# Performance work log

Measured on AMD Instinct MI355X. Metric: run time of the kernel, lower is better.

## Reference

```python
import jax, jax.numpy as jnp
import numpy as np

H_BINS = 64
SIGMA = 0.02
EPS = 1e-6


def setup_inputs() -> dict:
    key = jax.random.key(0)
    x = jax.random.uniform(key, (8, 3, 256, 256), dtype=jnp.float32)
    return {"x": x}


def reference(x):
    h = H_BINS
    L = x.shape[0]
    x = jnp.clip(x, 0.0, 1.0)
    I = x.reshape(L, 3, -1)                      # [L,3,N]
    Iy = jnp.sqrt(jnp.sum(I * I, axis=1) + EPS)  # [L,N] pixel intensity
    logs = jnp.log(I + EPS)                      # [L,3,N]
    # per-channel log-chromaticity: for c=0:(u=l0-l1, v=l0-l2); c=1:(l1-l0, l1-l2); c=2:(l2-l0, l2-l1)
    cu = jnp.array([1, 0, 0])
    cv = jnp.array([2, 2, 1])
    U = logs - logs[:, cu, :]                    # [L,3,N]
    V = logs - logs[:, cv, :]                    # [L,3,N]
    offset = jnp.linspace(-3.0, 3.0, h, dtype=jnp.float32)  # [h]
    inv_s2 = jnp.float32(1.0 / (SIGMA * SIGMA))
    # RBF-like (inverse-quadratic) soft binning kernels: [L,3,N,h]
    Ku = 1.0 / (1.0 + jnp.square(U[..., None] - offset) * inv_s2)
    Kv = 1.0 / (1.0 + jnp.square(V[..., None] - offset) * inv_s2)
    # weighted outer-product reduction over pixels -> [L,3,h,h]
    hists = jnp.einsum('ln,lcnu,lcnv->lcuv', Iy, Ku, Kv)
    # normalize each sample by its total mass
    total = jnp.sum(hists, axis=(1, 2, 3), keepdims=True)
    return hists / (total + EPS)
```

## Files before the change

kernel.cpp:

```cpp
#include <hip/hip_runtime.h>

#define H 64
#define NPIX 65536
#define LBATCH 8
#define LC 24
#define S_CHUNKS 32
#define PB 2048
#define EPSF 1e-6f
#define LN2_50 34.6573590f
#define NPART (LC * S_CHUNKS)
#define PART_FLOATS (NPART * H * H)

typedef _Float16 h8 __attribute__((ext_vector_type(8)));
typedef __fp16   g2 __attribute__((ext_vector_type(2)));
typedef float f32x16 __attribute__((ext_vector_type(16)));
union H8u { h8 v8; g2 v2[4]; };

#define KEV(d) __builtin_amdgcn_rcpf(fmaf((d), (d), 1.0f))
#define PK(a, b) __builtin_amdgcn_cvt_pkrtz((a), (b))

__global__ __launch_bounds__(256, 3) void hist_main(const float* __restrict__ x,
                                                    float* __restrict__ ws) {
    __shared__ float sU[PB];
    __shared__ float sV[PB];
    __shared__ float sW[PB];
    __shared__ float sHist[H * H];

    const int tid  = threadIdx.x;
    const int wv   = tid >> 6;
    const int lane = tid & 63;
    const int hf   = lane >> 5;
    const int ln   = lane & 31;
    const int lc   = blockIdx.y;
    const int l    = lc / 3;
    const int c    = lc - 3 * l;

    #pragma unroll
    for (int r = 0; r < 4; r++)
        *(float4*)&sHist[(r * 256 + tid) * 4] = make_float4(0.f, 0.f, 0.f, 0.f);

    const float* __restrict__ x0p = x + (l * 3 + 0) * NPIX;
    const float* __restrict__ x1p = x + (l * 3 + 1) * NPIX;
    const float* __restrict__ x2p = x + (l * 3 + 2) * NPIX;
    const int base = blockIdx.x * PB;

    #pragma unroll
    for (int pass = 0; pass < 2; pass++) {
        const int ploc = pass * 1024 + tid * 4;
        const float4 r0 = *(const float4*)&x0p[base + ploc];
        const float4 r1 = *(const float4*)&x1p[base + ploc];
        const float4 r2 = *(const float4*)&x2p[base + ploc];
        float4 U4, V4, W4;
        #define PREP(E) { \
            const float v0 = fminf(fmaxf(r0.E, 0.0f), 1.0f); \
            const float v1 = fminf(fmaxf(r1.E, 0.0f), 1.0f); \
            const float v2 = fminf(fmaxf(r2.E, 0.0f), 1.0f); \
            W4.E = __builtin_amdgcn_sqrtf(fmaf(v0, v0, fmaf(v1, v1, fmaf(v2, v2, EPSF)))); \
            const float lg0 = __builtin_amdgcn_logf(v0 + EPSF); \
            const float lg1 = __builtin_amdgcn_logf(v1 + EPSF); \
            const float lg2 = __builtin_amdgcn_logf(v2 + EPSF); \
            float U, V; \
            if (c == 0)      { U = lg0 - lg1; V = lg0 - lg2; } \
            else if (c == 1) { U = lg1 - lg0; V = lg1 - lg2; } \
            else             { U = lg2 - lg0; V = lg2 - lg1; } \
            U4.E = LN2_50 * U; V4.E = LN2_50 * V; }
        PREP(x) PREP(y) PREP(z) PREP(w)
        #undef PREP
        *(float4*)&sU[ploc] = U4;
        *(float4*)&sV[ploc] = V4;
        *(float4*)&sW[ploc] = W4;
    }
    __syncthreads();

    const float step50 = 50.0f * (6.0f / 63.0f);
    const float ou0 = -150.0f + step50 * (float)ln;
    const float ou1 = ou0 + step50 * 32.0f;

    f32x16 acc00, acc01, acc10, acc11;
    #pragma unroll
    for (int i = 0; i < 16; i++) { acc00[i] = 0.f; acc01[i] = 0.f; acc10[i] = 0.f; acc11[i] = 0.f; }

    const int wbase = wv * 512;
    #pragma unroll 2
    for (int ks = 0; ks < 32; ks++) {
        const int kb = wbase + ks * 16 + hf * 8;
        const float4 ua = *(const float4*)&sU[kb];
        const float4 ub = *(const float4*)&sU[kb + 4];
        const float4 va = *(const float4*)&sV[kb];
        const float4 vb = *(const float4*)&sV[kb + 4];
        const float4 wa = *(const float4*)&sW[kb];
        const float4 wb = *(const float4*)&sW[kb + 4];
        H8u A0, A1, B0, B1;
        A0.v2[0] = PK(wa.x * KEV(ua.x - ou0), wa.y * KEV(ua.y - ou0));
        A0.v2[1] = PK(wa.z * KEV(ua.z - ou0), wa.w * KEV(ua.w - ou0));
        A0.v2[2] = PK(wb.x * KEV(ub.x - ou0), wb.y * KEV(ub.y - ou0));
        A0.v2[3] = PK(wb.z * KEV(ub.z - ou0), wb.w * KEV(ub.w - ou0));
        A1.v2[0] = PK(wa.x * KEV(ua.x - ou1), wa.y * KEV(ua.y - ou1));
        A1.v2[1] = PK(wa.z * KEV(ua.z - ou1), wa.w * KEV(ua.w - ou1));
        A1.v2[2] = PK(wb.x * KEV(ub.x - ou1), wb.y * KEV(ub.y - ou1));
        A1.v2[3] = PK(wb.z * KEV(ub.z - ou1), wb.w * KEV(ub.w - ou1));
        B0.v2[0] = PK(KEV(va.x - ou0), KEV(va.y - ou0));
        B0.v2[1] = PK(KEV(va.z - ou0), KEV(va.w - ou0));
        B0.v2[2] = PK(KEV(vb.x - ou0), KEV(vb.y - ou0));
        B0.v2[3] = PK(KEV(vb.z - ou0), KEV(vb.w - ou0));
        B1.v2[0] = PK(KEV(va.x - ou1), KEV(va.y - ou1));
        B1.v2[1] = PK(KEV(va.z - ou1), KEV(va.w - ou1));
        B1.v2[2] = PK(KEV(vb.x - ou1), KEV(vb.y - ou1));
        B1.v2[3] = PK(KEV(vb.z - ou1), KEV(vb.w - ou1));
        acc00 = __builtin_amdgcn_mfma_f32_32x32x16_f16(A0.v8, B0.v8, acc00, 0, 0, 0);
        acc01 = __builtin_amdgcn_mfma_f32_32x32x16_f16(A0.v8, B1.v8, acc01, 0, 0, 0);
        acc10 = __builtin_amdgcn_mfma_f32_32x32x16_f16(A1.v8, B0.v8, acc10, 0, 0, 0);
        acc11 = __builtin_amdgcn_mfma_f32_32x32x16_f16(A1.v8, B1.v8, acc11, 0, 0, 0);
    }

    #pragma unroll
    for (int r = 0; r < 16; r++) {
        const int row = (r & 3) + 8 * (r >> 2) + 4 * hf;
        atomicAdd(&sHist[row * 64 + ln],             acc00[r]);
        atomicAdd(&sHist[row * 64 + 32 + ln],        acc01[r]);
        atomicAdd(&sHist[(row + 32) * 64 + ln],      acc10[r]);
        atomicAdd(&sHist[(row + 32) * 64 + 32 + ln], acc11[r]);
    }
    __syncthreads();

    float* __restrict__ g = ws + (lc * S_CHUNKS + blockIdx.x) * (H * H);
    #pragma unroll
    for (int r = 0; r < 4; r++) {
        const int i = (r * 256 + tid) * 4;
        *(float4*)&g[i] = *(const float4*)&sHist[i];
    }
}

__global__ __launch_bounds__(256) void hist_reduce(const float* __restrict__ ws,
                                                   float* __restrict__ out,
                                                   float* __restrict__ wsq) {
    const int lc  = blockIdx.x >> 2;
    const int off = (blockIdx.x & 3) * 1024 + threadIdx.x * 4;
    float4 a = make_float4(0.f, 0.f, 0.f, 0.f);
    #pragma unroll 8
    for (int ch = 0; ch < S_CHUNKS; ch++) {
        const float4 v = *(const float4*)&ws[(lc * S_CHUNKS + ch) * (H * H) + off];
        a.x += v.x; a.y += v.y; a.z += v.z; a.w += v.w;
    }
    *(float4*)&out[lc * (H * H) + off] = a;

    float s = (a.x + a.y) + (a.z + a.w);
    #pragma unroll
    for (int o = 32; o > 0; o >>= 1) s += __shfl_down(s, o, 64);
    __shared__ float ps[4];
    if ((threadIdx.x & 63) == 0) ps[threadIdx.x >> 6] = s;
    __syncthreads();
    if (threadIdx.x == 0) wsq[blockIdx.x] = (ps[0] + ps[1]) + (ps[2] + ps[3]);
}

__global__ __launch_bounds__(256) void hist_scale(float* __restrict__ out,
                                                  const float* __restrict__ wsq) {
    const int lc = blockIdx.x >> 2;
    const int l  = lc / 3;
    float T = 0.f;
    #pragma unroll
    for (int j = 0; j < 12; j++) T += wsq[l * 12 + j];
    const float inv = 1.0f / (T + EPSF);
    const int off = (blockIdx.x & 3) * 1024 + threadIdx.x * 4;
    float4 v = *(const float4*)&out[lc * (H * H) + off];
    v.x *= inv; v.y *= inv; v.z *= inv; v.w *= inv;
    *(float4*)&out[lc * (H * H) + off] = v;
}

extern "C" void kernel_launch(void* const* d_in, const int* in_sizes, int n_in,
                              void* d_out, int out_size, void* d_ws, size_t ws_size,
                              hipStream_t stream) {
    const float* x = (const float*)d_in[0];
    float* out = (float*)d_out;
    float* ws = (float*)d_ws;

    hipLaunchKernelGGL(hist_main,   dim3(S_CHUNKS, LC), dim3(256), 0, stream, x, ws);
    hipLaunchKernelGGL(hist_reduce, dim3(96),           dim3(256), 0, stream, ws, out, ws + PART_FLOATS);
    hipLaunchKernelGGL(hist_scale,  dim3(96),           dim3(256), 0, stream, out, ws + PART_FLOATS);
}
```

Measured before the change: 153.6 us.

## Template pixel chunk size, double the grid, alias LDS and prefetch K-step operands

Makes the per-block pixel chunk a template parameter and, when the workspace is large enough, launches 64 chunks of 1024 pixels per (sample, channel) instead of 32 of 2048. This doubles the number of blocks to fill more CUs and shortens each block's serial MFMA loop. The histogram scratch now aliases the U/V/W LDS buffers, so it is zeroed after the main loop behind an extra barrier, and shared-memory use per block drops. The inner loop also software-prefetches the next K-step's LDS operands and interleaves MFMA issue with kernel evaluation. The cost is twice as much partial-histogram traffic written and then read back by the reduce kernel.

```diff
diff --git a/kernel.cpp b/kernel.cpp
--- a/kernel.cpp
+++ b/kernel.cpp
@@ -4,12 +4,8 @@
 #define NPIX 65536
 #define LBATCH 8
 #define LC 24
-#define S_CHUNKS 32
-#define PB 2048
 #define EPSF 1e-6f
 #define LN2_50 34.6573590f
-#define NPART (LC * S_CHUNKS)
-#define PART_FLOATS (NPART * H * H)
 
 typedef _Float16 h8 __attribute__((ext_vector_type(8)));
 typedef __fp16   g2 __attribute__((ext_vector_type(2)));
@@ -19,12 +15,14 @@
 #define KEV(d) __builtin_amdgcn_rcpf(fmaf((d), (d), 1.0f))
 #define PK(a, b) __builtin_amdgcn_cvt_pkrtz((a), (b))
 
+template <int PBT>
 __global__ __launch_bounds__(256, 3) void hist_main(const float* __restrict__ x,
                                                     float* __restrict__ ws) {
-    __shared__ float sU[PB];
-    __shared__ float sV[PB];
-    __shared__ float sW[PB];
-    __shared__ float sHist[H * H];
+    constexpr int SB = (3 * PBT > H * H) ? 3 * PBT : H * H;
+    __shared__ float sBuf[SB];
+    float* const sU = sBuf;
+    float* const sV = sBuf + PBT;
+    float* const sW = sBuf + 2 * PBT;
 
     const int tid  = threadIdx.x;
     const int wv   = tid >> 6;
@@ -35,17 +33,13 @@
     const int l    = lc / 3;
     const int c    = lc - 3 * l;
 
-    #pragma unroll
-    for (int r = 0; r < 4; r++)
-        *(float4*)&sHist[(r * 256 + tid) * 4] = make_float4(0.f, 0.f, 0.f, 0.f);
-
     const float* __restrict__ x0p = x + (l * 3 + 0) * NPIX;
     const float* __restrict__ x1p = x + (l * 3 + 1) * NPIX;
     const float* __restrict__ x2p = x + (l * 3 + 2) * NPIX;
-    const int base = blockIdx.x * PB;
-
-    #pragma unroll
-    for (int pass = 0; pass < 2; pass++) {
+    const int base = blockIdx.x * PBT;
+
+    #pragma unroll
+    for (int pass = 0; pass < PBT / 1024; pass++) {
         const int ploc = pass * 1024 + tid * 4;
         const float4 r0 = *(const float4*)&x0p[base + ploc];
         const float4 r1 = *(const float4*)&x1p[base + ploc];
@@ -80,66 +74,85 @@
     #pragma unroll
     for (int i = 0; i < 16; i++) { acc00[i] = 0.f; acc01[i] = 0.f; acc10[i] = 0.f; acc11[i] = 0.f; }
 
-    const int wbase = wv * 512;
+    const int wbase = wv * (PBT / 4);
+    constexpr int KSTEPS = PBT / 64;
+
+    float4 cua, cub, cva, cvb, cwa, cwb;
+    float4 pua, pub, pva, pvb, pwa, pwb;
+
+    #define LOADK(P, ks) { const int kb = wbase + (ks) * 16 + hf * 8; \
+        P##ua = *(const float4*)&sU[kb]; P##ub = *(const float4*)&sU[kb + 4]; \
+        P##va = *(const float4*)&sV[kb]; P##vb = *(const float4*)&sV[kb + 4]; \
+        P##wa = *(const float4*)&sW[kb]; P##wb = *(const float4*)&sW[kb + 4]; }
+
+    #define BODY() { H8u A0, A1, B0, B1; \
+        A0.v2[0] = PK(cwa.x * KEV(cua.x - ou0), cwa.y * KEV(cua.y - ou0)); \
+        A0.v2[1] = PK(cwa.z * KEV(cua.z - ou0), cwa.w * KEV(cua.w - ou0)); \
+        A0.v2[2] = PK(cwb.x * KEV(cub.x - ou0), cwb.y * KEV(cub.y - ou0)); \
+        A0.v2[3] = PK(cwb.z * KEV(cub.z - ou0), cwb.w * KEV(cub.w - ou0)); \
+        B0.v2[0] = PK(KEV(cva.x - ou0), KEV(cva.y - ou0)); \
+        B0.v2[1] = PK(KEV(cva.z - ou0), KEV(cva.w - ou0)); \
+        B0.v2[2] = PK(KEV(cvb.x - ou0), KEV(cvb.y - ou0)); \
+        B0.v2[3] = PK(KEV(cvb.z - ou0), KEV(cvb.w - ou0)); \
+        acc00 = __builtin_amdgcn_mfma_f32_32x32x16_f16(A0.v8, B0.v8, acc00, 0, 0, 0); \
+        A1.v2[0] = PK(cwa.x * KEV(cua.x - ou1), cwa.y * KEV(cua.y - ou1)); \
+        A1.v2[1] = PK(cwa.z * KEV(cua.z - ou1), cwa.w * KEV(cua.w - ou1)); \
+        A1.v2[2] = PK(cwb.x * KEV(cub.x - ou1), cwb.y * KEV(cub.y - ou1)); \
+        A1.v2[3] = PK(cwb.z * KEV(cub.z - ou1), cwb.w * KEV(cub.w - ou1)); \
+        acc10 = __builtin_amdgcn_mfma_f32_32x32x16_f16(A1.v8, B0.v8, acc10, 0, 0, 0); \
+        B1.v2[0] = PK(KEV(cva.x - ou1), KEV(cva.y - ou1)); \
+        B1.v2[1] = PK(KEV(cva.z - ou1), KEV(cva.w - ou1)); \
+        B1.v2[2] = PK(KEV(cvb.x - ou1), KEV(cvb.y - ou1)); \
+        B1.v2[3] = PK(KEV(cvb.z - ou1), KEV(cvb.w - ou1)); \
+        acc01 = __builtin_amdgcn_mfma_f32_32x32x16_f16(A0.v8, B1.v8, acc01, 0, 0, 0); \
+        acc11 = __builtin_amdgcn_mfma_f32_32x32x16_f16(A1.v8, B1.v8, acc11, 0, 0, 0); }
+
+    LOADK(c, 0)
     #pragma unroll 2
-    for (int ks = 0; ks < 32; ks++) {
-        const int kb = wbase + ks * 16 + hf * 8;
-        const float4 ua = *(const float4*)&sU[kb];
-        const float4 ub = *(const float4*)&sU[kb + 4];
-        const float4 va = *(const float4*)&sV[kb];
-        const float4 vb = *(const float4*)&sV[kb + 4];
-        const float4 wa = *(const float4*)&sW[kb];
-        const float4 wb = *(const float4*)&sW[kb + 4];
-        H8u A0, A1, B0, B1;
-        A0.v2[0] = PK(wa.x * KEV(ua.x - ou0), wa.y * KEV(ua.y - ou0));
-        A0.v2[1] = PK(wa.z * KEV(ua.z - ou0), wa.w * KEV(ua.w - ou0));
-        A0.v2[2] = PK(wb.x * KEV(ub.x - ou0), wb.y * KEV(ub.y - ou0));
-        A0.v2[3] = PK(wb.z * KEV(ub.z - ou0), wb.w * KEV(ub.w - ou0));
-        A1.v2[0] = PK(wa.x * KEV(ua.x - ou1), wa.y * KEV(ua.y - ou1));
-        A1.v2[1] = PK(wa.z * KEV(ua.z - ou1), wa.w * KEV(ua.w - ou1));
-        A1.v2[2] = PK(wb.x * KEV(ub.x - ou1), wb.y * KEV(ub.y - ou1));
-        A1.v2[3] = PK(wb.z * KEV(ub.z - ou1), wb.w * KEV(ub.w - ou1));
-        B0.v2[0] = PK(KEV(va.x - ou0), KEV(va.y - ou0));
-        B0.v2[1] = PK(KEV(va.z - ou0), KEV(va.w - ou0));
-        B0.v2[2] = PK(KEV(vb.x - ou0), KEV(vb.y - ou0));
-        B0.v2[3] = PK(KEV(vb.z - ou0), KEV(vb.w - ou0));
-        B1.v2[0] = PK(KEV(va.x - ou1), KEV(va.y - ou1));
-        B1.v2[1] = PK(KEV(va.z - ou1), KEV(va.w - ou1));
-        B1.v2[2] = PK(KEV(vb.x - ou1), KEV(vb.y - ou1));
-        B1.v2[3] = PK(KEV(vb.z - ou1), KEV(vb.w - ou1));
-        acc00 = __builtin_amdgcn_mfma_f32_32x32x16_f16(A0.v8, B0.v8, acc00, 0, 0, 0);
-        acc01 = __builtin_amdgcn_mfma_f32_32x32x16_f16(A0.v8, B1.v8, acc01, 0, 0, 0);
-        acc10 = __builtin_amdgcn_mfma_f32_32x32x16_f16(A1.v8, B0.v8, acc10, 0, 0, 0);
-        acc11 = __builtin_amdgcn_mfma_f32_32x32x16_f16(A1.v8, B1.v8, acc11, 0, 0, 0);
-    }
+    for (int ks = 0; ks < KSTEPS - 1; ks++) {
+        LOADK(p, ks + 1)
+        BODY()
+        cua = pua; cub = pub; cva = pva; cvb = pvb; cwa = pwa; cwb = pwb;
+    }
+    BODY()
+    #undef LOADK
+    #undef BODY
+
+    __syncthreads();
+
+    #pragma unroll
+    for (int r = 0; r < H * H / 1024; r++)
+        *(float4*)&sBuf[(r * 256 + tid) * 4] = make_float4(0.f, 0.f, 0.f, 0.f);
+    __syncthreads();
 
     #pragma unroll
     for (int r = 0; r < 16; r++) {
         const int row = (r & 3) + 8 * (r >> 2) + 4 * hf;
-        atomicAdd(&sHist[row * 64 + ln],             acc00[r]);
-        atomicAdd(&sHist[row * 64 + 32 + ln],        acc01[r]);
-        atomicAdd(&sHist[(row + 32) * 64 + ln],      acc10[r]);
-        atomicAdd(&sHist[(row + 32) * 64 + 32 + ln], acc11[r]);
-    }
-    __syncthreads();
-
-    float* __restrict__ g = ws + (lc * S_CHUNKS + blockIdx.x) * (H * H);
+        atomicAdd(&sBuf[row * 64 + ln],             acc00[r]);
+        atomicAdd(&sBuf[row * 64 + 32 + ln],        acc01[r]);
+        atomicAdd(&sBuf[(row + 32) * 64 + ln],      acc10[r]);
+        atomicAdd(&sBuf[(row + 32) * 64 + 32 + ln], acc11[r]);
+    }
+    __syncthreads();
+
+    float* __restrict__ g = ws + (blockIdx.y * gridDim.x + blockIdx.x) * (H * H);
     #pragma unroll
     for (int r = 0; r < 4; r++) {
         const int i = (r * 256 + tid) * 4;
-        *(float4*)&g[i] = *(const float4*)&sHist[i];
+        *(float4*)&g[i] = *(const float4*)&sBuf[i];
     }
 }
 
 __global__ __launch_bounds__(256) void hist_reduce(const float* __restrict__ ws,
                                                    float* __restrict__ out,
-                                                   float* __restrict__ wsq) {
+                                                   float* __restrict__ wsq,
+                                                   int nch) {
     const int lc  = blockIdx.x >> 2;
     const int off = (blockIdx.x & 3) * 1024 + threadIdx.x * 4;
     float4 a = make_float4(0.f, 0.f, 0.f, 0.f);
     #pragma unroll 8
-    for (int ch = 0; ch < S_CHUNKS; ch++) {
-        const float4 v = *(const float4*)&ws[(lc * S_CHUNKS + ch) * (H * H) + off];
+    for (int ch = 0; ch < nch; ch++) {
+        const float4 v = *(const float4*)&ws[(lc * nch + ch) * (H * H) + off];
         a.x += v.x; a.y += v.y; a.z += v.z; a.w += v.w;
     }
     *(float4*)&out[lc * (H * H) + off] = a;
@@ -174,7 +187,16 @@
     float* out = (float*)d_out;
     float* ws = (float*)d_ws;
 
-    hipLaunchKernelGGL(hist_main,   dim3(S_CHUNKS, LC), dim3(256), 0, stream, x, ws);
-    hipLaunchKernelGGL(hist_reduce, dim3(96),           dim3(256), 0, stream, ws, out, ws + PART_FLOATS);
-    hipLaunchKernelGGL(hist_scale,  dim3(96),           dim3(256), 0, stream, out, ws + PART_FLOATS);
-}
+    const size_t need64 = ((size_t)64 * LC * H * H + 96) * sizeof(float);
+    if (ws_size >= need64) {
+        float* wsq = ws + (size_t)64 * LC * H * H;
+        hipLaunchKernelGGL(hist_main<1024>, dim3(64, LC), dim3(256), 0, stream, x, ws);
+        hipLaunchKernelGGL(hist_reduce,     dim3(96),     dim3(256), 0, stream, ws, out, wsq, 64);
+        hipLaunchKernelGGL(hist_scale,      dim3(96),     dim3(256), 0, stream, out, wsq);
+    } else {
+        float* wsq = ws + (size_t)32 * LC * H * H;
+        hipLaunchKernelGGL(hist_main<2048>, dim3(32, LC), dim3(256), 0, stream, x, ws);
+        hipLaunchKernelGGL(hist_reduce,     dim3(96),     dim3(256), 0, stream, ws, out, wsq, 32);
+        hipLaunchKernelGGL(hist_scale,      dim3(96),     dim3(256), 0, stream, out, wsq);
+    }
+}
```

After: 218.9 us. +42.5%, slower.
